# Kernel tuning notes

Hardware: AMD Instinct MI355X
Metric: run time of the kernel (lower is better)

Reference implementation:

```python
import jax, jax.numpy as jnp
import numpy as np

B, S, D, H = 2, 2048, 1024, 16
DK = D // H
SOFTCAP = 30.0


def setup_inputs() -> dict:
    key = jax.random.key(0)
    ks = jax.random.split(key, 6)
    inp = jax.random.normal(ks[0], (B, S, D), dtype=jnp.float32)
    count_bias = jax.random.normal(ks[1], (B, 1, S, S), dtype=jnp.float32) * 0.1
    # causal boolean mask: True = allowed
    causal = jnp.tril(jnp.ones((S, S), dtype=bool))
    attn_mask = jnp.broadcast_to(causal[None, None, :, :], (B, 1, S, S))
    scale = 0.02
    Wq = jax.random.normal(ks[2], (D, D), dtype=jnp.float32) * scale
    Wk = jax.random.normal(ks[3], (D, D), dtype=jnp.float32) * scale
    Wv = jax.random.normal(ks[4], (D, D), dtype=jnp.float32) * scale
    Wo = jax.random.normal(ks[5], (D, D), dtype=jnp.float32) * scale
    return {"inp": inp, "count_bias": count_bias, "attn_mask": attn_mask,
            "Wq": Wq, "Wk": Wk, "Wv": Wv, "Wo": Wo}


def reference(inp, count_bias, attn_mask, Wq, Wk, Wv, Wo):
    b = inp.shape[0]
    # nn.Linear: y = x @ W.T ; reshape to (B, H, S, DK)
    def proj(x, W):
        return jnp.einsum('bsd,ed->bse', x, W).reshape(b, -1, H, DK).transpose(0, 2, 1, 3)
    q = proj(inp, Wq)
    k = proj(inp, Wk)
    v = proj(inp, Wv)
    scale = 1.0 / np.sqrt(DK).astype(np.float32)
    scores = jnp.einsum('bhqd,bhkd->bhqk', q, k) * scale  # (B,H,S,S)
    scores = scores + count_bias  # broadcast over heads
    scores = jnp.tanh(scores / SOFTCAP) * SOFTCAP  # softcap > 0
    scores = jnp.where(attn_mask, scores, -jnp.inf)
    weights = jax.nn.softmax(scores, axis=-1)
    o = jnp.einsum('bhqk,bhkd->bhqd', weights, v)
    o = o.transpose(0, 2, 1, 3).reshape(b, -1, D)
    out = jnp.einsum('bsd,ed->bse', o, Wo)
    return out
```

## Files before the change

### kernel.cpp

```cpp
#include <hip/hip_runtime.h>
#include <hip/hip_bf16.h>

#define GK 1024

typedef __attribute__((ext_vector_type(8))) short bf16x8;
typedef __attribute__((ext_vector_type(4))) float f32x4;
typedef __attribute__((ext_vector_type(16))) float f32x16;
typedef __attribute__((ext_vector_type(4))) unsigned short ushort4v;

__device__ __forceinline__ f32x4 mfma16(bf16x8 a, bf16x8 b, f32x4 c) {
  return __builtin_amdgcn_mfma_f32_16x16x32_bf16(a, b, c, 0, 0, 0);
}
__device__ __forceinline__ f32x16 mfma32(bf16x8 a, bf16x8 b, f32x16 c) {
  return __builtin_amdgcn_mfma_f32_32x32x16_bf16(a, b, c, 0, 0, 0);
}

__device__ __forceinline__ unsigned short f2b(float f) {
  union { float f; unsigned int u; } x; x.f = f;
  return (unsigned short)((x.u + 0x7fffu + ((x.u >> 16) & 1u)) >> 16);
}

__device__ __forceinline__ unsigned int pk2(float lo, float hi) {
  float2 f; f.x = lo; f.y = hi;
  __hip_bfloat162 t = __float22bfloat162_rn(f);
  union { __hip_bfloat162 b; unsigned int u; } c; c.b = t;
  return c.u;
}

__device__ __forceinline__ float fexp2(float x) {
#if __has_builtin(__builtin_amdgcn_exp2f)
  return __builtin_amdgcn_exp2f(x);
#else
  return exp2f(x);
#endif
}
__device__ __forceinline__ float frcp(float x) {
#if __has_builtin(__builtin_amdgcn_rcpf)
  return __builtin_amdgcn_rcpf(x);
#else
  return 1.0f / x;
#endif
}

__device__ __forceinline__ void gl_lds16(const void* g, void* l) {
  __builtin_amdgcn_global_load_lds(
      (const __attribute__((address_space(1))) unsigned int*)g,
      (__attribute__((address_space(3))) unsigned int*)l, 16, 0, 0);
}

__global__ __launch_bounds__(256) void convert_kernel(
    const float* __restrict__ inp,
    const float* __restrict__ wq, const float* __restrict__ wk,
    const float* __restrict__ wv, const float* __restrict__ wo,
    unsigned short* __restrict__ Xb, unsigned short* __restrict__ Wcat)
{
  const size_t XN = (size_t)4194304;
  size_t i = ((size_t)blockIdx.x * 256 + threadIdx.x) * 4;
  const float* src; unsigned short* dst; size_t off;
  if (i < XN) {
    src = inp; dst = Xb; off = i;
  } else {
    size_t j = i - XN;
    int w = (int)(j >> 20);
    off = j & 1048575u;
    src = (w == 0) ? wq : (w == 1) ? wk : (w == 2) ? wv : wo;
    dst = Wcat + ((size_t)w << 20);
  }
  f32x4 v = *(const f32x4*)(src + off);
  ushort4v o;
#pragma unroll
  for (int t = 0; t < 4; ++t) o[t] = f2b(v[t]);
  *(ushort4v*)(dst + off) = o;
}

__device__ __forceinline__ void gemm_mainloop(
    const unsigned short* __restrict__ A, const unsigned short* __restrict__ Wt,
    int m0, int n0, int tid, unsigned short* As, unsigned short* Bs,
    f32x4 (&acc)[4][4])
{
  const int lane = tid & 63;
  const int wave = tid >> 6;
  const int wr = wave >> 1, wc = wave & 1;
  const int lq = lane & 15, g = lane >> 4;

  const int r_in = lane >> 2;
  const int c8 = (lane & 3) * 8;

  const unsigned short* Ap0 = A + (size_t)(m0 + wave * 32 + r_in) * GK + c8;
  const unsigned short* Ap1 = Ap0 + (size_t)16 * GK;
  const unsigned short* Wp0 = Wt + (size_t)(n0 + wave * 32 + r_in) * GK + c8;
  const unsigned short* Wp1 = Wp0 + (size_t)16 * GK;
  unsigned short* As0 = As + wave * 1024;
  unsigned short* Bs0 = Bs + wave * 1024;

  for (int kt = 0; kt < GK / 32; ++kt) {
    const int k0 = kt * 32;
    __syncthreads();
    gl_lds16(Ap0 + k0, As0);
    gl_lds16(Ap1 + k0, As0 + 512);
    gl_lds16(Wp0 + k0, Bs0);
    gl_lds16(Wp1 + k0, Bs0 + 512);
    __syncthreads();
    bf16x8 af[4], bfr[4];
#pragma unroll
    for (int i = 0; i < 4; ++i)
      af[i] = *(const bf16x8*)(As + (wr * 64 + i * 16 + lq) * 32 + g * 8);
#pragma unroll
    for (int j = 0; j < 4; ++j)
      bfr[j] = *(const bf16x8*)(Bs + (wc * 64 + j * 16 + lq) * 32 + g * 8);
#pragma unroll
    for (int i = 0; i < 4; ++i)
#pragma unroll
      for (int j = 0; j < 4; ++j)
        acc[i][j] = mfma16(af[i], bfr[j], acc[i][j]);
  }
}

__global__ __launch_bounds__(256) void gemm_qkv(
    const unsigned short* __restrict__ X, const unsigned short* __restrict__ Wcat,
    unsigned short* __restrict__ Qb, unsigned short* __restrict__ Kb,
    unsigned short* __restrict__ Vt)
{
  __shared__ unsigned short As[4096];
  __shared__ unsigned short Bs[4096];
  f32x4 acc[4][4];
#pragma unroll
  for (int i = 0; i < 4; ++i)
#pragma unroll
    for (int j = 0; j < 4; ++j) acc[i][j] = (f32x4){0.f, 0.f, 0.f, 0.f};

  const int z = blockIdx.z;
  const int m0 = blockIdx.x * 128, n0 = blockIdx.y * 128;
  gemm_mainloop(X, Wcat + ((size_t)z << 20), m0, n0, (int)threadIdx.x, As, Bs, acc);

  const int lane = threadIdx.x & 63;
  const int wave = threadIdx.x >> 6;
  const int wr = wave >> 1, wc = wave & 1, lq = lane & 15, g = lane >> 4;

  if (z < 2) {
    unsigned short* C = z ? Kb : Qb;
#pragma unroll
    for (int i = 0; i < 4; ++i)
#pragma unroll
      for (int j = 0; j < 4; ++j) {
        int col = n0 + wc * 64 + j * 16 + lq;
#pragma unroll
        for (int r = 0; r < 4; ++r) {
          int row = m0 + wr * 64 + i * 16 + g * 4 + r;
          C[(size_t)row * 1024 + col] = f2b(acc[i][j][r]);
        }
      }
  } else {
#pragma unroll
    for (int i = 0; i < 4; ++i)
#pragma unroll
      for (int j = 0; j < 4; ++j) {
        int col = n0 + wc * 64 + j * 16 + lq;
        int row0 = m0 + wr * 64 + i * 16 + g * 4;
        int b = row0 >> 11;
        int s = row0 & 2047;
        ushort4v pv;
#pragma unroll
        for (int r = 0; r < 4; ++r) pv[r] = f2b(acc[i][j][r]);
        *(ushort4v*)(Vt + (size_t)(b * 1024 + col) * 2048 + s) = pv;
      }
  }
}

__global__ __launch_bounds__(256) void gemm_out(
    const unsigned short* __restrict__ Ob, const unsigned short* __restrict__ Wo,
    float* __restrict__ out)
{
  __shared__ unsigned short As[4096];
  __shared__ unsigned short Bs[4096];
  f32x4 acc[4][4];
#pragma unroll
  for (int i = 0; i < 4; ++i)
#pragma unroll
    for (int j = 0; j < 4; ++j) acc[i][j] = (f32x4){0.f, 0.f, 0.f, 0.f};

  const int m0 = blockIdx.x * 128, n0 = blockIdx.y * 128;
  gemm_mainloop(Ob, Wo, m0, n0, (int)threadIdx.x, As, Bs, acc);

  const int lane = threadIdx.x & 63;
  const int wave = threadIdx.x >> 6;
  const int wr = wave >> 1, wc = wave & 1, lq = lane & 15, g = lane >> 4;
#pragma unroll
  for (int i = 0; i < 4; ++i)
#pragma unroll
    for (int j = 0; j < 4; ++j) {
      int col = n0 + wc * 64 + j * 16 + lq;
#pragma unroll
      for (int r = 0; r < 4; ++r) {
        int row = m0 + wr * 64 + i * 16 + g * 4 + r;
        out[(size_t)row * 1024 + col] = acc[i][j][r];
      }
    }
}

__device__ __forceinline__ void attn_chain(
    const bf16x8 (&qf)[4], const f32x4 (&bvs)[4],
    bf16x8 kf0, bf16x8 kf1, bf16x8 kf2, bf16x8 kf3,
    bf16x8 va00, bf16x8 va01, bf16x8 va10, bf16x8 va11,
    bool msk, int ql, int hi,
    f32x16& o0, f32x16& o1, float& pls)
{
  const float INV30 = 0.033333333333f;
  const float C3 = -0.333333333f, C5 = 0.133333333f;
  const float C1 = 43.28085122666891f;

  f32x16 st = {0.f,0.f,0.f,0.f,0.f,0.f,0.f,0.f,0.f,0.f,0.f,0.f,0.f,0.f,0.f,0.f};
  st = mfma32(kf0, qf[0], st);
  st = mfma32(kf1, qf[1], st);
  st = mfma32(kf2, qf[2], st);
  st = mfma32(kf3, qf[3], st);

  float p[16];
#pragma unroll
  for (int reg = 0; reg < 16; ++reg) {
    float v = fmaf(st[reg], 0.125f, bvs[reg >> 2][reg & 3]);
    float y = v * INV30;
    float y2 = y * y;
    float t = y * fmaf(y2, fmaf(y2, C5, C3), 1.0f);
    p[reg] = fexp2(fmaf(t, C1, -C1));
  }
  if (msk) {
#pragma unroll
    for (int reg = 0; reg < 16; ++reg) {
      int krow = (reg & 3) + 8 * (reg >> 2) + 4 * hi;
      p[reg] = (krow <= ql) ? p[reg] : 0.f;
    }
  }
  float a0 = (p[0] + p[1]) + (p[2] + p[3]);
  float a1 = (p[4] + p[5]) + (p[6] + p[7]);
  float a2 = (p[8] + p[9]) + (p[10] + p[11]);
  float a3 = (p[12] + p[13]) + (p[14] + p[15]);
  pls += (a0 + a1) + (a2 + a3);

  unsigned int wv[8];
#pragma unroll
  for (int j = 0; j < 8; ++j) wv[j] = pk2(p[2 * j], p[2 * j + 1]);
  unsigned int x0 = hi ? wv[0] : wv[2], x1 = hi ? wv[1] : wv[3];
  x0 = __shfl_xor(x0, 32); x1 = __shfl_xor(x1, 32);
  unsigned int y0 = hi ? wv[4] : wv[6], y1 = hi ? wv[5] : wv[7];
  y0 = __shfl_xor(y0, 32); y1 = __shfl_xor(y1, 32);
  union { unsigned int u[4]; bf16x8 v; } B0, B1;
  B0.u[0] = hi ? x0 : wv[0]; B0.u[1] = hi ? x1 : wv[1];
  B0.u[2] = hi ? wv[2] : x0; B0.u[3] = hi ? wv[3] : x1;
  B1.u[0] = hi ? y0 : wv[4]; B1.u[1] = hi ? y1 : wv[5];
  B1.u[2] = hi ? wv[6] : y0; B1.u[3] = hi ? wv[7] : y1;

  o0 = mfma32(va00, B0.v, o0);
  o0 = mfma32(va01, B1.v, o0);
  o1 = mfma32(va10, B0.v, o1);
  o1 = mfma32(va11, B1.v, o1);
}

__global__ __launch_bounds__(256, 2) void attn_fwd(
    const unsigned short* __restrict__ Qb, const unsigned short* __restrict__ Kb,
    const unsigned short* __restrict__ Vt, const float* __restrict__ bias,
    unsigned short* __restrict__ Ob)
{
  __shared__ __attribute__((aligned(16))) unsigned char lds[65536];

  const int tid = (int)threadIdx.x;
  const int lane = tid & 63;
  const int w = tid >> 6;
  const int bid = (int)blockIdx.x;
  const int bh = (bid & 7) * 4 + ((bid >> 3) & 3);
  const int qp = bid >> 5;
  const int b = bh >> 4, h = bh & 15;
  const int tA = qp, tB = 63 - qp;
  const int q0A = tA * 32, q0B = tB * 32;
  const int ql = lane & 31;
  const int hi = lane >> 5;

  const unsigned short* QpA = Qb + (size_t)(b * 2048 + q0A + ql) * 1024 + h * 64 + 8 * hi;
  const unsigned short* QpB = Qb + (size_t)(b * 2048 + q0B + ql) * 1024 + h * 64 + 8 * hi;
  bf16x8 qfA[4], qfB[4];
#pragma unroll
  for (int c = 0; c < 4; ++c) {
    qfA[c] = *(const bf16x8*)(QpA + 16 * c);
    qfB[c] = *(const bf16x8*)(QpB + 16 * c);
  }

  const unsigned short* KsrcL = Kb + (size_t)(b * 2048 + (lane >> 3)) * 1024
                                + h * 64 + (((lane & 7) ^ ((lane >> 3) & 7)) << 3);
  const unsigned short* VsrcL = Vt + (size_t)(bh * 64 + (lane >> 2)) * 2048
                                + (((lane & 3) ^ ((lane >> 2) & 3)) << 3);
  unsigned char* const KdstW = lds + w * 16384;
  unsigned char* const VdstW = lds + w * 16384 + 8192;

  const float* BpA = bias + (size_t)b * 4194304 + (size_t)(q0A + ql) * 2048 + 4 * hi;
  const float* BpB = bias + (size_t)b * 4194304 + (size_t)(q0B + ql) * 2048 + 4 * hi;

  float plsA = 0.f, plsB = 0.f;
  f32x16 oA0 = {0.f,0.f,0.f,0.f,0.f,0.f,0.f,0.f,0.f,0.f,0.f,0.f,0.f,0.f,0.f,0.f};
  f32x16 oA1 = oA0, oB0 = oA0, oB1 = oA0;

  auto stageKV = [&](int kt, int db) {
#pragma unroll
    for (int j = 0; j < 4; ++j)
      gl_lds16(KsrcL + (size_t)kt * 32768 + j * 8192, KdstW + db * 4096 + j * 1024);
#pragma unroll
    for (int j = 0; j < 4; ++j)
      gl_lds16(VsrcL + (size_t)j * 32768 + kt * 32, VdstW + db * 4096 + j * 1024);
  };

  stageKV(w, 0);
  int db = 0;
  for (int kt0 = 0; kt0 <= tB; kt0 += 4) {
    const int mykt = kt0 + w;
    asm volatile("s_waitcnt vmcnt(0)" ::: "memory");
    __builtin_amdgcn_sched_barrier(0);
    if (mykt + 4 <= tB) stageKV(mykt + 4, db ^ 1);
    __builtin_amdgcn_sched_barrier(0);

    if (mykt <= tB) {
      const unsigned char* Ksh = lds + w * 16384 + db * 4096;
      const unsigned char* Vsh = lds + w * 16384 + 8192 + db * 4096;
      bf16x8 kf[4];
#pragma unroll
      for (int c = 0; c < 4; ++c)
        kf[c] = *(const bf16x8*)(Ksh + ql * 128 + (((hi + 2 * c) ^ (ql & 7)) << 4));
      const int vb = ((ql >> 4) << 10) + ((ql & 15) << 6);
      bf16x8 va00 = *(const bf16x8*)(Vsh + vb + (((hi) ^ (ql & 3)) << 4));
      bf16x8 va01 = *(const bf16x8*)(Vsh + vb + (((hi + 2) ^ (ql & 3)) << 4));
      bf16x8 va10 = *(const bf16x8*)(Vsh + 2048 + vb + (((hi) ^ (ql & 3)) << 4));
      bf16x8 va11 = *(const bf16x8*)(Vsh + 2048 + vb + (((hi + 2) ^ (ql & 3)) << 4));

      f32x4 bvsB[4];
#pragma unroll
      for (int j = 0; j < 4; ++j) bvsB[j] = *(const f32x4*)(BpB + mykt * 32 + 8 * j);
      attn_chain(qfB, bvsB, kf[0], kf[1], kf[2], kf[3], va00, va01, va10, va11,
                 mykt == tB, ql, hi, oB0, oB1, plsB);
      if (mykt <= tA) {
        f32x4 bvsA[4];
#pragma unroll
        for (int j = 0; j < 4; ++j) bvsA[j] = *(const f32x4*)(BpA + mykt * 32 + 8 * j);
        attn_chain(qfA, bvsA, kf[0], kf[1], kf[2], kf[3], va00, va01, va10, va11,
                   mykt == tA, ql, hi, oA0, oA1, plsA);
      }
    }
    db ^= 1;
  }

  __syncthreads();
  float* ldsF = (float*)lds;
  float* lsumbuf = ldsF + 8448;
  float* rowinv = ldsF + 8960;
  lsumbuf[(w * 2 + hi) * 32 + ql] = plsA;
  lsumbuf[256 + (w * 2 + hi) * 32 + ql] = plsB;
  if (w >= 2) {
    float* OA = ldsF + (w - 2) * 2112;
    float* OB = ldsF + (2 + (w - 2)) * 2112;
#pragma unroll
    for (int reg = 0; reg < 16; ++reg) {
      int d0 = (reg & 3) + 8 * (reg >> 2) + 4 * hi;
      OA[d0 * 33 + ql] = oA0[reg];
      OA[(d0 + 32) * 33 + ql] = oA1[reg];
      OB[d0 * 33 + ql] = oB0[reg];
      OB[(d0 + 32) * 33 + ql] = oB1[reg];
    }
  }
  __syncthreads();
  if (w < 2) {
    float* OA = ldsF + w * 2112;
    float* OB = ldsF + (2 + w) * 2112;
#pragma unroll
    for (int reg = 0; reg < 16; ++reg) {
      int d0 = (reg & 3) + 8 * (reg >> 2) + 4 * hi;
      OA[d0 * 33 + ql] += oA0[reg];
      OA[(d0 + 32) * 33 + ql] += oA1[reg];
      OB[d0 * 33 + ql] += oB0[reg];
      OB[(d0 + 32) * 33 + ql] += oB1[reg];
    }
  }
  __syncthreads();
  if (tid < 64) {
    int t = tid >> 5, q = tid & 31;
    float s = 0.f;
#pragma unroll
    for (int j = 0; j < 8; ++j) s += lsumbuf[t * 256 + j * 32 + q];
    rowinv[t * 32 + q] = frcp(s);
  }
  __syncthreads();
#pragma unroll
  for (int it = 0; it < 16; ++it) {
    int i = it * 256 + tid;
    int t = i >> 11;
    int rem = i & 2047;
    int q = rem >> 6, d = rem & 63;
    float val = (ldsF[t * 4224 + d * 33 + q] + ldsF[t * 4224 + 2112 + d * 33 + q])
                * rowinv[t * 32 + q];
    int row = b * 2048 + (t ? q0B : q0A) + q;
    Ob[(size_t)row * 1024 + h * 64 + d] = f2b(val);
  }
}

extern "C" void kernel_launch(void* const* d_in, const int* in_sizes, int n_in,
                              void* d_out, int out_size, void* d_ws, size_t ws_size,
                              hipStream_t stream) {
  (void)in_sizes; (void)n_in; (void)out_size; (void)ws_size;
  const float* inp  = (const float*)d_in[0];
  const float* bias = (const float*)d_in[1];
  const float* wq = (const float*)d_in[3];
  const float* wk = (const float*)d_in[4];
  const float* wv = (const float*)d_in[5];
  const float* wo = (const float*)d_in[6];
  float* out = (float*)d_out;

  unsigned short* Xb   = (unsigned short*)d_ws;
  unsigned short* Wcat = Xb + 4194304;
  unsigned short* Qb   = Wcat + 4194304;
  unsigned short* Kb   = Qb + 4194304;
  unsigned short* Vt   = Kb + 4194304;
  unsigned short* Ob   = Vt + 4194304;

  convert_kernel<<<8192, 256, 0, stream>>>(inp, wq, wk, wv, wo, Xb, Wcat);
  gemm_qkv<<<dim3(32, 8, 3), dim3(256), 0, stream>>>(Xb, Wcat, Qb, Kb, Vt);
  attn_fwd<<<1024, 256, 0, stream>>>(Qb, Kb, Vt, bias, Ob);
  gemm_out<<<dim3(32, 8, 1), dim3(256), 0, stream>>>(Ob, Wcat + 3 * 1048576, out);
}
```

Measured before the change: 140.5 us.

## Share staged K/V tiles across two query-tile groups in 512-thread attention blocks

The attention kernel now runs 512-thread blocks made of two groups of four waves. Each group handles its own balanced pair of causal query tiles, while one shared, double-buffered set of K/V tiles staged in LDS feeds both groups. This halves the grid and the global K/V loads per query tile. In exchange the per-wave explicit vmcnt waits are replaced by block-wide barriers on every iteration, and the loop always runs its full trip count. The tighter launch bounds of (512, 4) may also cap VGPRs and cause spills.

```diff
diff --git a/kernel.cpp b/kernel.cpp
--- a/kernel.cpp
+++ b/kernel.cpp
@@ -256,21 +256,24 @@
   o1 = mfma32(va11, B1.v, o1);
 }
 
-__global__ __launch_bounds__(256, 2) void attn_fwd(
+__global__ __launch_bounds__(512, 4) void attn_fwd(
     const unsigned short* __restrict__ Qb, const unsigned short* __restrict__ Kb,
     const unsigned short* __restrict__ Vt, const float* __restrict__ bias,
     unsigned short* __restrict__ Ob)
 {
-  __shared__ __attribute__((aligned(16))) unsigned char lds[65536];
+  __shared__ __attribute__((aligned(16))) unsigned char lds[73728];
 
   const int tid = (int)threadIdx.x;
   const int lane = tid & 63;
   const int w = tid >> 6;
+  const int ph = w & 3;
+  const int grp = w >> 2;
   const int bid = (int)blockIdx.x;
   const int bh = (bid & 7) * 4 + ((bid >> 3) & 3);
   const int qp = bid >> 5;
   const int b = bh >> 4, h = bh & 15;
-  const int tA = qp, tB = 63 - qp;
+  const int tA = grp ? (31 - qp) : qp;
+  const int tB = grp ? (32 + qp) : (63 - qp);
   const int q0A = tA * 32, q0B = tB * 32;
   const int ql = lane & 31;
   const int hi = lane >> 5;
@@ -288,8 +291,6 @@
                                 + h * 64 + (((lane & 7) ^ ((lane >> 3) & 7)) << 3);
   const unsigned short* VsrcL = Vt + (size_t)(bh * 64 + (lane >> 2)) * 2048
                                 + (((lane & 3) ^ ((lane >> 2) & 3)) << 3);
-  unsigned char* const KdstW = lds + w * 16384;
-  unsigned char* const VdstW = lds + w * 16384 + 8192;
 
   const float* BpA = bias + (size_t)b * 4194304 + (size_t)(q0A + ql) * 2048 + 4 * hi;
   const float* BpB = bias + (size_t)b * 4194304 + (size_t)(q0B + ql) * 2048 + 4 * hi;
@@ -299,26 +300,27 @@
   f32x16 oA1 = oA0, oB0 = oA0, oB1 = oA0;
 
   auto stageKV = [&](int kt, int db) {
+    unsigned char* Kd = lds + ph * 16384 + db * 8192;
+    unsigned char* Vd = Kd + 4096;
 #pragma unroll
     for (int j = 0; j < 4; ++j)
-      gl_lds16(KsrcL + (size_t)kt * 32768 + j * 8192, KdstW + db * 4096 + j * 1024);
+      gl_lds16(KsrcL + (size_t)kt * 32768 + j * 8192, Kd + j * 1024);
 #pragma unroll
     for (int j = 0; j < 4; ++j)
-      gl_lds16(VsrcL + (size_t)j * 32768 + kt * 32, VdstW + db * 4096 + j * 1024);
+      gl_lds16(VsrcL + (size_t)j * 32768 + kt * 32, Vd + j * 1024);
   };
 
-  stageKV(w, 0);
+  if (w < 4) stageKV(ph, 0);
+  __syncthreads();
+
   int db = 0;
-  for (int kt0 = 0; kt0 <= tB; kt0 += 4) {
-    const int mykt = kt0 + w;
-    asm volatile("s_waitcnt vmcnt(0)" ::: "memory");
-    __builtin_amdgcn_sched_barrier(0);
-    if (mykt + 4 <= tB) stageKV(mykt + 4, db ^ 1);
-    __builtin_amdgcn_sched_barrier(0);
+  for (int kt0 = 0; kt0 < 64; kt0 += 4) {
+    const int mykt = kt0 + ph;
+    if (w < 4 && mykt + 4 <= tB) stageKV(mykt + 4, db ^ 1);
 
     if (mykt <= tB) {
-      const unsigned char* Ksh = lds + w * 16384 + db * 4096;
-      const unsigned char* Vsh = lds + w * 16384 + 8192 + db * 4096;
+      const unsigned char* Ksh = lds + ph * 16384 + db * 8192;
+      const unsigned char* Vsh = Ksh + 4096;
       bf16x8 kf[4];
 #pragma unroll
       for (int c = 0; c < 4; ++c)
@@ -342,18 +344,19 @@
                    mykt == tA, ql, hi, oA0, oA1, plsA);
       }
     }
+    __syncthreads();
     db ^= 1;
   }
 
-  __syncthreads();
-  float* ldsF = (float*)lds;
-  float* lsumbuf = ldsF + 8448;
-  float* rowinv = ldsF + 8960;
-  lsumbuf[(w * 2 + hi) * 32 + ql] = plsA;
-  lsumbuf[256 + (w * 2 + hi) * 32 + ql] = plsB;
-  if (w >= 2) {
-    float* OA = ldsF + (w - 2) * 2112;
-    float* OB = ldsF + (2 + (w - 2)) * 2112;
+  float* G = (float*)lds + grp * 9216;
+  float* lsumbuf = G + 8448;
+  float* rowinv = G + 8960;
+  const int gw = w & 3;
+  lsumbuf[(gw * 2 + hi) * 32 + ql] = plsA;
+  lsumbuf[256 + (gw * 2 + hi) * 32 + ql] = plsB;
+  if (gw >= 2) {
+    float* OA = G + (0 * 2 + (gw - 2)) * 2112;
+    float* OB = G + (1 * 2 + (gw - 2)) * 2112;
 #pragma unroll
     for (int reg = 0; reg < 16; ++reg) {
       int d0 = (reg & 3) + 8 * (reg >> 2) + 4 * hi;
@@ -364,9 +367,9 @@
     }
   }
   __syncthreads();
-  if (w < 2) {
-    float* OA = ldsF + w * 2112;
-    float* OB = ldsF + (2 + w) * 2112;
+  if (gw < 2) {
+    float* OA = G + (0 * 2 + gw) * 2112;
+    float* OB = G + (1 * 2 + gw) * 2112;
 #pragma unroll
     for (int reg = 0; reg < 16; ++reg) {
       int d0 = (reg & 3) + 8 * (reg >> 2) + 4 * hi;
@@ -377,8 +380,9 @@
     }
   }
   __syncthreads();
-  if (tid < 64) {
-    int t = tid >> 5, q = tid & 31;
+  const int gtid = tid & 255;
+  if (gtid < 64) {
+    int t = gtid >> 5, q = gtid & 31;
     float s = 0.f;
 #pragma unroll
     for (int j = 0; j < 8; ++j) s += lsumbuf[t * 256 + j * 32 + q];
@@ -387,11 +391,11 @@
   __syncthreads();
 #pragma unroll
   for (int it = 0; it < 16; ++it) {
-    int i = it * 256 + tid;
+    int i = it * 256 + gtid;
     int t = i >> 11;
     int rem = i & 2047;
     int q = rem >> 6, d = rem & 63;
-    float val = (ldsF[t * 4224 + d * 33 + q] + ldsF[t * 4224 + 2112 + d * 33 + q])
+    float val = (G[(t * 2 + 0) * 2112 + d * 33 + q] + G[(t * 2 + 1) * 2112 + d * 33 + q])
                 * rowinv[t * 32 + q];
     int row = b * 2048 + (t ? q0B : q0A) + q;
     Ob[(size_t)row * 1024 + h * 64 + d] = f2b(val);
@@ -419,6 +423,6 @@
 
   convert_kernel<<<8192, 256, 0, stream>>>(inp, wq, wk, wv, wo, Xb, Wcat);
   gemm_qkv<<<dim3(32, 8, 3), dim3(256), 0, stream>>>(Xb, Wcat, Qb, Kb, Vt);
-  attn_fwd<<<1024, 256, 0, stream>>>(Qb, Kb, Vt, bias, Ob);
+  attn_fwd<<<512, 512, 0, stream>>>(Qb, Kb, Vt, bias, Ob);
   gemm_out<<<dim3(32, 8, 1), dim3(256), 0, stream>>>(Ob, Wcat + 3 * 1048576, out);
 }
```

Result: slower. 244.1 us (+73.7%).

## Double-buffer GEMM LDS tiles; single-buffer attention KV to raise occupancy

Applied to the files above, without the earlier changes.

The shared GEMM main loop now double-buffers its A/B LDS tiles, prefetching the next k-tile before computing the current one and using one barrier per iteration instead of two. The attention kernel goes the other way: it drops its KV double buffer, shrinks LDS, and raises launch bounds from 2 to 4 blocks per CU. It also issues the bias loads before waiting on the KV copy. The aim is to hide GEMM global latency and to cover attention latency through more resident waves. The cost is twice the LDS in the GEMM kernels and no per-wave prefetch overlap in attention, plus tighter register limits there.

```diff
diff --git a/kernel.cpp b/kernel.cpp
--- a/kernel.cpp
+++ b/kernel.cpp
@@ -90,29 +90,36 @@
   const unsigned short* Ap1 = Ap0 + (size_t)16 * GK;
   const unsigned short* Wp0 = Wt + (size_t)(n0 + wave * 32 + r_in) * GK + c8;
   const unsigned short* Wp1 = Wp0 + (size_t)16 * GK;
-  unsigned short* As0 = As + wave * 1024;
-  unsigned short* Bs0 = Bs + wave * 1024;
-
+
+  auto stage = [&](int kt, int d) {
+    const int k0 = kt * 32;
+    gl_lds16(Ap0 + k0, As + d * 4096 + wave * 1024);
+    gl_lds16(Ap1 + k0, As + d * 4096 + wave * 1024 + 512);
+    gl_lds16(Wp0 + k0, Bs + d * 4096 + wave * 1024);
+    gl_lds16(Wp1 + k0, Bs + d * 4096 + wave * 1024 + 512);
+  };
+
+  stage(0, 0);
+  __syncthreads();
+  int d = 0;
   for (int kt = 0; kt < GK / 32; ++kt) {
-    const int k0 = kt * 32;
-    __syncthreads();
-    gl_lds16(Ap0 + k0, As0);
-    gl_lds16(Ap1 + k0, As0 + 512);
-    gl_lds16(Wp0 + k0, Bs0);
-    gl_lds16(Wp1 + k0, Bs0 + 512);
-    __syncthreads();
+    if (kt + 1 < GK / 32) stage(kt + 1, d ^ 1);
+    const unsigned short* Asb = As + d * 4096;
+    const unsigned short* Bsb = Bs + d * 4096;
     bf16x8 af[4], bfr[4];
 #pragma unroll
     for (int i = 0; i < 4; ++i)
-      af[i] = *(const bf16x8*)(As + (wr * 64 + i * 16 + lq) * 32 + g * 8);
+      af[i] = *(const bf16x8*)(Asb + (wr * 64 + i * 16 + lq) * 32 + g * 8);
 #pragma unroll
     for (int j = 0; j < 4; ++j)
-      bfr[j] = *(const bf16x8*)(Bs + (wc * 64 + j * 16 + lq) * 32 + g * 8);
+      bfr[j] = *(const bf16x8*)(Bsb + (wc * 64 + j * 16 + lq) * 32 + g * 8);
 #pragma unroll
     for (int i = 0; i < 4; ++i)
 #pragma unroll
       for (int j = 0; j < 4; ++j)
         acc[i][j] = mfma16(af[i], bfr[j], acc[i][j]);
+    __syncthreads();
+    d ^= 1;
   }
 }
 
@@ -121,8 +128,8 @@
     unsigned short* __restrict__ Qb, unsigned short* __restrict__ Kb,
     unsigned short* __restrict__ Vt)
 {
-  __shared__ unsigned short As[4096];
-  __shared__ unsigned short Bs[4096];
+  __shared__ unsigned short As[8192];
+  __shared__ unsigned short Bs[8192];
   f32x4 acc[4][4];
 #pragma unroll
   for (int i = 0; i < 4; ++i)
@@ -171,8 +178,8 @@
     const unsigned short* __restrict__ Ob, const unsigned short* __restrict__ Wo,
     float* __restrict__ out)
 {
-  __shared__ unsigned short As[4096];
-  __shared__ unsigned short Bs[4096];
+  __shared__ unsigned short As[8192];
+  __shared__ unsigned short Bs[8192];
   f32x4 acc[4][4];
 #pragma unroll
   for (int i = 0; i < 4; ++i)
@@ -256,12 +263,12 @@
   o1 = mfma32(va11, B1.v, o1);
 }
 
-__global__ __launch_bounds__(256, 2) void attn_fwd(
+__global__ __launch_bounds__(256, 4) void attn_fwd(
     const unsigned short* __restrict__ Qb, const unsigned short* __restrict__ Kb,
     const unsigned short* __restrict__ Vt, const float* __restrict__ bias,
     unsigned short* __restrict__ Ob)
 {
-  __shared__ __attribute__((aligned(16))) unsigned char lds[65536];
+  __shared__ __attribute__((aligned(16))) unsigned char lds[36352];
 
   const int tid = (int)threadIdx.x;
   const int lane = tid & 63;
@@ -288,8 +295,8 @@
                                 + h * 64 + (((lane & 7) ^ ((lane >> 3) & 7)) << 3);
   const unsigned short* VsrcL = Vt + (size_t)(bh * 64 + (lane >> 2)) * 2048
                                 + (((lane & 3) ^ ((lane >> 2) & 3)) << 3);
-  unsigned char* const KdstW = lds + w * 16384;
-  unsigned char* const VdstW = lds + w * 16384 + 8192;
+  unsigned char* const Kdst = lds + w * 8192;
+  unsigned char* const Vdst = Kdst + 4096;
 
   const float* BpA = bias + (size_t)b * 4194304 + (size_t)(q0A + ql) * 2048 + 4 * hi;
   const float* BpB = bias + (size_t)b * 4194304 + (size_t)(q0B + ql) * 2048 + 4 * hi;
@@ -298,51 +305,47 @@
   f32x16 oA0 = {0.f,0.f,0.f,0.f,0.f,0.f,0.f,0.f,0.f,0.f,0.f,0.f,0.f,0.f,0.f,0.f};
   f32x16 oA1 = oA0, oB0 = oA0, oB1 = oA0;
 
-  auto stageKV = [&](int kt, int db) {
+  auto stageKV = [&](int kt) {
 #pragma unroll
     for (int j = 0; j < 4; ++j)
-      gl_lds16(KsrcL + (size_t)kt * 32768 + j * 8192, KdstW + db * 4096 + j * 1024);
+      gl_lds16(KsrcL + (size_t)kt * 32768 + j * 8192, Kdst + j * 1024);
 #pragma unroll
     for (int j = 0; j < 4; ++j)
-      gl_lds16(VsrcL + (size_t)j * 32768 + kt * 32, VdstW + db * 4096 + j * 1024);
+      gl_lds16(VsrcL + (size_t)j * 32768 + kt * 32, Vdst + j * 1024);
   };
 
-  stageKV(w, 0);
-  int db = 0;
-  for (int kt0 = 0; kt0 <= tB; kt0 += 4) {
-    const int mykt = kt0 + w;
+  for (int kt = w; kt <= tB; kt += 4) {
+    __builtin_amdgcn_sched_barrier(0);
+    stageKV(kt);
+    const bool doA = (kt <= tA);
+    f32x4 bvsB[4], bvsA[4];
+#pragma unroll
+    for (int j = 0; j < 4; ++j) bvsB[j] = *(const f32x4*)(BpB + kt * 32 + 8 * j);
+    if (doA) {
+#pragma unroll
+      for (int j = 0; j < 4; ++j) bvsA[j] = *(const f32x4*)(BpA + kt * 32 + 8 * j);
+    }
     asm volatile("s_waitcnt vmcnt(0)" ::: "memory");
     __builtin_amdgcn_sched_barrier(0);
-    if (mykt + 4 <= tB) stageKV(mykt + 4, db ^ 1);
-    __builtin_amdgcn_sched_barrier(0);
-
-    if (mykt <= tB) {
-      const unsigned char* Ksh = lds + w * 16384 + db * 4096;
-      const unsigned char* Vsh = lds + w * 16384 + 8192 + db * 4096;
-      bf16x8 kf[4];
-#pragma unroll
-      for (int c = 0; c < 4; ++c)
-        kf[c] = *(const bf16x8*)(Ksh + ql * 128 + (((hi + 2 * c) ^ (ql & 7)) << 4));
-      const int vb = ((ql >> 4) << 10) + ((ql & 15) << 6);
-      bf16x8 va00 = *(const bf16x8*)(Vsh + vb + (((hi) ^ (ql & 3)) << 4));
-      bf16x8 va01 = *(const bf16x8*)(Vsh + vb + (((hi + 2) ^ (ql & 3)) << 4));
-      bf16x8 va10 = *(const bf16x8*)(Vsh + 2048 + vb + (((hi) ^ (ql & 3)) << 4));
-      bf16x8 va11 = *(const bf16x8*)(Vsh + 2048 + vb + (((hi + 2) ^ (ql & 3)) << 4));
-
-      f32x4 bvsB[4];
-#pragma unroll
-      for (int j = 0; j < 4; ++j) bvsB[j] = *(const f32x4*)(BpB + mykt * 32 + 8 * j);
-      attn_chain(qfB, bvsB, kf[0], kf[1], kf[2], kf[3], va00, va01, va10, va11,
-                 mykt == tB, ql, hi, oB0, oB1, plsB);
-      if (mykt <= tA) {
-        f32x4 bvsA[4];
-#pragma unroll
-        for (int j = 0; j < 4; ++j) bvsA[j] = *(const f32x4*)(BpA + mykt * 32 + 8 * j);
-        attn_chain(qfA, bvsA, kf[0], kf[1], kf[2], kf[3], va00, va01, va10, va11,
-                   mykt == tA, ql, hi, oA0, oA1, plsA);
-      }
-    }
-    db ^= 1;
+
+    const unsigned char* Ksh = Kdst;
+    const unsigned char* Vsh = Vdst;
+    bf16x8 kf[4];
+#pragma unroll
+    for (int c = 0; c < 4; ++c)
+      kf[c] = *(const bf16x8*)(Ksh + ql * 128 + (((hi + 2 * c) ^ (ql & 7)) << 4));
+    const int vb = ((ql >> 4) << 10) + ((ql & 15) << 6);
+    bf16x8 va00 = *(const bf16x8*)(Vsh + vb + (((hi) ^ (ql & 3)) << 4));
+    bf16x8 va01 = *(const bf16x8*)(Vsh + vb + (((hi + 2) ^ (ql & 3)) << 4));
+    bf16x8 va10 = *(const bf16x8*)(Vsh + 2048 + vb + (((hi) ^ (ql & 3)) << 4));
+    bf16x8 va11 = *(const bf16x8*)(Vsh + 2048 + vb + (((hi + 2) ^ (ql & 3)) << 4));
+
+    attn_chain(qfB, bvsB, kf[0], kf[1], kf[2], kf[3], va00, va01, va10, va11,
+               kt == tB, ql, hi, oB0, oB1, plsB);
+    if (doA) {
+      attn_chain(qfA, bvsA, kf[0], kf[1], kf[2], kf[3], va00, va01, va10, va11,
+                 kt == tA, ql, hi, oA0, oA1, plsA);
+    }
   }
 
   __syncthreads();
```

New measurement: 252.2 us. +79.4%, slower.

## Prefetch bias before staging next KV tile and wait only on current tile

Applied to the files above, without the earlier changes.

Issues the count_bias global loads for the current key tile at the top of each iteration, before the async global-to-LDS loads for the next K/V tile. It then waits with vmcnt(8) so only the current tile's loads must complete, instead of draining every outstanding load. The LDS layout moves so each double-buffer slot holds K and V next to each other. The intent is to overlap bias and next-tile fetch latency with compute; the change depends on the counted wait matching the number of loads actually issued.

```diff
diff --git a/kernel.cpp b/kernel.cpp
--- a/kernel.cpp
+++ b/kernel.cpp
@@ -289,7 +289,6 @@
   const unsigned short* VsrcL = Vt + (size_t)(bh * 64 + (lane >> 2)) * 2048
                                 + (((lane & 3) ^ ((lane >> 2) & 3)) << 3);
   unsigned char* const KdstW = lds + w * 16384;
-  unsigned char* const VdstW = lds + w * 16384 + 8192;
 
   const float* BpA = bias + (size_t)b * 4194304 + (size_t)(q0A + ql) * 2048 + 4 * hi;
   const float* BpB = bias + (size_t)b * 4194304 + (size_t)(q0B + ql) * 2048 + 4 * hi;
@@ -299,48 +298,54 @@
   f32x16 oA1 = oA0, oB0 = oA0, oB1 = oA0;
 
   auto stageKV = [&](int kt, int db) {
+    unsigned char* Kd = KdstW + db * 8192;
+    unsigned char* Vd = Kd + 4096;
 #pragma unroll
     for (int j = 0; j < 4; ++j)
-      gl_lds16(KsrcL + (size_t)kt * 32768 + j * 8192, KdstW + db * 4096 + j * 1024);
+      gl_lds16(KsrcL + (size_t)kt * 32768 + j * 8192, Kd + j * 1024);
 #pragma unroll
     for (int j = 0; j < 4; ++j)
-      gl_lds16(VsrcL + (size_t)j * 32768 + kt * 32, VdstW + db * 4096 + j * 1024);
+      gl_lds16(VsrcL + (size_t)j * 32768 + kt * 32, Vd + j * 1024);
   };
 
   stageKV(w, 0);
   int db = 0;
-  for (int kt0 = 0; kt0 <= tB; kt0 += 4) {
-    const int mykt = kt0 + w;
-    asm volatile("s_waitcnt vmcnt(0)" ::: "memory");
+  for (int kt = w; kt <= tB; kt += 4) {
+    const bool doA = (kt <= tA);
+    f32x4 bvsB[4], bvsA[4];
+#pragma unroll
+    for (int j = 0; j < 4; ++j) bvsB[j] = *(const f32x4*)(BpB + kt * 32 + 8 * j);
+    if (doA) {
+#pragma unroll
+      for (int j = 0; j < 4; ++j) bvsA[j] = *(const f32x4*)(BpA + kt * 32 + 8 * j);
+    }
     __builtin_amdgcn_sched_barrier(0);
-    if (mykt + 4 <= tB) stageKV(mykt + 4, db ^ 1);
+    const bool hasNext = (kt + 4 <= tB);
+    if (hasNext) {
+      stageKV(kt + 4, db ^ 1);
+      asm volatile("s_waitcnt vmcnt(8)" ::: "memory");
+    } else {
+      asm volatile("s_waitcnt vmcnt(0)" ::: "memory");
+    }
     __builtin_amdgcn_sched_barrier(0);
 
-    if (mykt <= tB) {
-      const unsigned char* Ksh = lds + w * 16384 + db * 4096;
-      const unsigned char* Vsh = lds + w * 16384 + 8192 + db * 4096;
-      bf16x8 kf[4];
-#pragma unroll
-      for (int c = 0; c < 4; ++c)
-        kf[c] = *(const bf16x8*)(Ksh + ql * 128 + (((hi + 2 * c) ^ (ql & 7)) << 4));
-      const int vb = ((ql >> 4) << 10) + ((ql & 15) << 6);
-      bf16x8 va00 = *(const bf16x8*)(Vsh + vb + (((hi) ^ (ql & 3)) << 4));
-      bf16x8 va01 = *(const bf16x8*)(Vsh + vb + (((hi + 2) ^ (ql & 3)) << 4));
-      bf16x8 va10 = *(const bf16x8*)(Vsh + 2048 + vb + (((hi) ^ (ql & 3)) << 4));
-      bf16x8 va11 = *(const bf16x8*)(Vsh + 2048 + vb + (((hi + 2) ^ (ql & 3)) << 4));
-
-      f32x4 bvsB[4];
-#pragma unroll
-      for (int j = 0; j < 4; ++j) bvsB[j] = *(const f32x4*)(BpB + mykt * 32 + 8 * j);
-      attn_chain(qfB, bvsB, kf[0], kf[1], kf[2], kf[3], va00, va01, va10, va11,
-                 mykt == tB, ql, hi, oB0, oB1, plsB);
-      if (mykt <= tA) {
-        f32x4 bvsA[4];
-#pragma unroll
-        for (int j = 0; j < 4; ++j) bvsA[j] = *(const f32x4*)(BpA + mykt * 32 + 8 * j);
-        attn_chain(qfA, bvsA, kf[0], kf[1], kf[2], kf[3], va00, va01, va10, va11,
-                   mykt == tA, ql, hi, oA0, oA1, plsA);
-      }
+    const unsigned char* Ksh = KdstW + db * 8192;
+    const unsigned char* Vsh = Ksh + 4096;
+    bf16x8 kf[4];
+#pragma unroll
+    for (int c = 0; c < 4; ++c)
+      kf[c] = *(const bf16x8*)(Ksh + ql * 128 + (((hi + 2 * c) ^ (ql & 7)) << 4));
+    const int vb = ((ql >> 4) << 10) + ((ql & 15) << 6);
+    bf16x8 va00 = *(const bf16x8*)(Vsh + vb + (((hi) ^ (ql & 3)) << 4));
+    bf16x8 va01 = *(const bf16x8*)(Vsh + vb + (((hi + 2) ^ (ql & 3)) << 4));
+    bf16x8 va10 = *(const bf16x8*)(Vsh + 2048 + vb + (((hi) ^ (ql & 3)) << 4));
+    bf16x8 va11 = *(const bf16x8*)(Vsh + 2048 + vb + (((hi + 2) ^ (ql & 3)) << 4));
+
+    attn_chain(qfB, bvsB, kf[0], kf[1], kf[2], kf[3], va00, va01, va10, va11,
+               kt == tB, ql, hi, oB0, oB1, plsB);
+    if (doA) {
+      attn_chain(qfA, bvsA, kf[0], kf[1], kf[2], kf[3], va00, va01, va10, va11,
+                 kt == tA, ql, hi, oA0, oA1, plsA);
     }
     db ^= 1;
   }
```

New measurement: 146.4 us. 1.04x slower.
